# Optimization experiments

Hardware: AMD Instinct MI355X
Metric: run time of the kernel (lower is better)

The kernel has to match this reference:

```python
import jax, jax.numpy as jnp
import numpy as np

NEG_SLOPE = 0.2
CONV3_NUM, CONV1_NUM, POLY_NUM = 3, 5, 4
FEAT_DIM = CONV3_NUM * 84 + CONV1_NUM * 12 + POLY_NUM * 12  # 360
DN = ('NCHW', 'OIHW', 'NCHW')


def leaky_relu(x):
    return jnp.where(x >= 0, x, NEG_SLOPE * x)


def conv3x3(x, feat):
    # per-sample dynamic 3x3 conv: feat[:, :81] -> kernel [3,3,3,3], feat[:, 81:84] -> bias
    B = x.shape[0]
    k = feat[:, :81].reshape(B, 3, 3, 3, 3)
    b = feat[:, 81:84]

    def one(xi, ki, bi):
        y = jax.lax.conv_general_dilated(xi[None], ki, (1, 1), 'SAME', dimension_numbers=DN)[0]
        return y + bi[:, None, None]

    return leaky_relu(jax.vmap(one)(x, k, b))


def conv1x1(x, feat):
    B = x.shape[0]
    k = feat[:, :9].reshape(B, 3, 3, 1, 1)
    b = feat[:, 9:12]

    def one(xi, ki, bi):
        y = jax.lax.conv_general_dilated(xi[None], ki, (1, 1), 'VALID', dimension_numbers=DN)[0]
        return y + bi[:, None, None]

    return leaky_relu(jax.vmap(one)(x, k, b))


def conv_stack(x, feature):
    residual = x
    for i in range(CONV3_NUM):
        x = conv3x3(x, feature[:, i * 84:(i + 1) * 84])
    off = CONV3_NUM * 84
    for i in range(CONV1_NUM):
        x = conv1x1(x, feature[:, off + i * 12:off + (i + 1) * 12])
    return residual + x


def att_map(feat, h_mat, w_mat, xc):
    # product over POLY_NUM of (a*h + b*w + c*x + d)
    att = jnp.ones_like(xc)
    for i in range(POLY_NUM):
        a = feat[:, i * 4 + 0].reshape(-1, 1, 1, 1)
        b = feat[:, i * 4 + 1].reshape(-1, 1, 1, 1)
        c = feat[:, i * 4 + 2].reshape(-1, 1, 1, 1)
        d = feat[:, i * 4 + 3].reshape(-1, 1, 1, 1)
        att = att * (a * h_mat + b * w_mat + c * xc + d)
    return att


def apply_attention(x, feature):
    H, W = x.shape[2], x.shape[3]
    h_mat = (jnp.arange(H, dtype=x.dtype) / H).reshape(1, 1, H, 1)
    w_mat = (jnp.arange(W, dtype=x.dtype) / W).reshape(1, 1, 1, W)
    off = CONV3_NUM * 84 + CONV1_NUM * 12
    atts = [att_map(feature[:, off + c * POLY_NUM * 4: off + (c + 1) * POLY_NUM * 4],
                    h_mat, w_mat, x[:, c:c + 1]) for c in range(3)]  # R, G, B
    att = jnp.concatenate(atts, axis=1)
    return x * (1 + att)


def setup_inputs() -> dict:
    key = jax.random.key(0)
    k1, k2, k3 = jax.random.split(key, 3)
    x = jax.random.uniform(k1, (8, 3, 512, 512), dtype=jnp.float32)
    thumb_x = jax.random.uniform(k2, (8, 3, 64, 64), dtype=jnp.float32)
    Wm = jax.random.normal(k3, (3, FEAT_DIM), dtype=jnp.float32) * 0.05
    bm = jnp.zeros((FEAT_DIM,), dtype=jnp.float32)
    return {"x": x, "thumb_x": thumb_x, "Wm": Wm, "bm": bm}


def reference(x, thumb_x, Wm, bm):
    # meta: GAP over thumbnail -> linear -> per-sample hypernetwork features [B, 360]
    feature = jnp.mean(thumb_x, axis=(2, 3)) @ Wm + bm
    x = conv_stack(x, feature)
    x = apply_attention(x, feature)
    thumb = conv_stack(thumb_x, feature)
    thumb = apply_attention(thumb, feature)
    return (x, thumb)
```

## Files before the change

### kernel.cpp

```cpp
#include <hip/hip_runtime.h>


typedef float v2f __attribute__((ext_vector_type(2)));
#define FMA2(a, b, c) __builtin_elementwise_fma((a), (b), (c))

__device__ __forceinline__ v2f leaky2(v2f v) {
    return __builtin_elementwise_max(v, v * 0.2f);
}

constexpr int STRD = 84;
constexpr int ROWS0 = 22;
constexpr int CHS  = ROWS0 * STRD;
constexpr int BUFSZ = 3 * CHS + 16;

__global__ __launch_bounds__(384) void prep_kernel(
    const float* __restrict__ thumb, const float* __restrict__ Wm,
    const float* __restrict__ bm, float* __restrict__ feat)
{
    const int b = blockIdx.x;
    const int t = threadIdx.x;
    const int ch = t >> 7;
    const int l  = t & 127;
    const float4* p = (const float4*)(thumb + (size_t)b * 3 * 4096);
    float s = 0.f;
#pragma unroll
    for (int k = 0; k < 8; ++k) {
        float4 v = p[ch * 1024 + l + k * 128];
        s += v.x + v.y + v.z + v.w;
    }
    __shared__ float red[384];
    red[t] = s;
    __syncthreads();
    for (int off = 64; off > 0; off >>= 1) {
        if (l < off) red[t] += red[t + off];
        __syncthreads();
    }
    if (t < 360) {
        const float sc = 1.f / 4096.f;
        const float m0 = red[0] * sc, m1 = red[128] * sc, m2 = red[256] * sc;
        feat[b * 360 + t] =
            fmaf(m0, Wm[t], fmaf(m1, Wm[360 + t], fmaf(m2, Wm[720 + t], bm[t])));
    }
}

__device__ __forceinline__ void conv_rows_pk(
    const float* __restrict__ buf, const float* __restrict__ fw,
    int r0, int gx, v2f acc[3][4])
{
    const float b0 = fw[81], b1 = fw[82], b2 = fw[83];
#pragma unroll
    for (int c = 0; c < 4; ++c) {
        v2f i0 = {b0, b0}; v2f i1 = {b1, b1}; v2f i2 = {b2, b2};
        acc[0][c] = i0; acc[1][c] = i1; acc[2][c] = i2;
    }
    const int gA = (gx < 0) ? 0 : gx;
#pragma unroll
    for (int ich = 0; ich < 3; ++ich) {
        float4 QA[4], QB[4], QC[4];
#pragma unroll
        for (int ri = 0; ri < 4; ++ri) {
            const int idx = ich * CHS + (r0 + 2 + ri) * STRD;
            QA[ri] = *(const float4*)&buf[idx + gA];
            QB[ri] = *(const float4*)&buf[idx + gx + 4];
            QC[ri] = *(const float4*)&buf[idx + gx + 8];
        }
#pragma unroll
        for (int dy = 0; dy < 3; ++dy) {
            v2f win[6];
            {
                v2f a = {QA[dy].w, QA[dy + 1].w}; win[0] = a;
                v2f b = {QB[dy].x, QB[dy + 1].x}; win[1] = b;
                v2f c = {QB[dy].y, QB[dy + 1].y}; win[2] = c;
                v2f d = {QB[dy].z, QB[dy + 1].z}; win[3] = d;
                v2f e = {QB[dy].w, QB[dy + 1].w}; win[4] = e;
                v2f f = {QC[dy].x, QC[dy + 1].x}; win[5] = f;
            }
#pragma unroll
            for (int oc = 0; oc < 3; ++oc) {
                const float w0 = fw[oc * 27 + ich * 9 + dy * 3 + 0];
                const float w1 = fw[oc * 27 + ich * 9 + dy * 3 + 1];
                const float w2 = fw[oc * 27 + ich * 9 + dy * 3 + 2];
                v2f W0 = {w0, w0}; v2f W1 = {w1, w1}; v2f W2 = {w2, w2};
#pragma unroll
                for (int c = 0; c < 4; ++c) {
                    acc[oc][c] = FMA2(win[c], W0,
                                 FMA2(win[c + 1], W1,
                                 FMA2(win[c + 2], W2, acc[oc][c])));
                }
            }
        }
    }
}

__device__ __forceinline__ void write_strip_pk(
    float* __restrict__ buf, int r0, int gx, v2f acc[3][4])
{
#pragma unroll
    for (int oc = 0; oc < 3; ++oc) {
        v2f l0 = leaky2(acc[oc][0]);
        v2f l1 = leaky2(acc[oc][1]);
        v2f l2 = leaky2(acc[oc][2]);
        v2f l3 = leaky2(acc[oc][3]);
        float4 ra = make_float4(l0.x, l1.x, l2.x, l3.x);
        float4 rb = make_float4(l0.y, l1.y, l2.y, l3.y);
        *(float4*)&buf[oc * CHS + (r0 + 3) * STRD + gx + 4] = ra;
        *(float4*)&buf[oc * CHS + (r0 + 4) * STRD + gx + 4] = rb;
    }
}

__global__ __launch_bounds__(256, 4) void conv_att_kernel(
    const float* __restrict__ x, const float* __restrict__ thumb,
    const float* __restrict__ feat, float* __restrict__ out)
{
    __shared__ float buf[BUFSZ];

    int id = blockIdx.x;
    const float* src; float* dst; int H, W, b, trow, tcol;
    if (id < 2048) {
        b = id >> 8; const int t = id & 255;
        H = 512; W = 512; trow = (t >> 3) * 16; tcol = (t & 7) * 64;
        src = x; dst = out;
    } else {
        const int i2 = id - 2048;
        b = i2 >> 2; trow = (i2 & 3) * 16; tcol = 0;
        H = 64; W = 64; src = thumb;
        dst = out + (size_t)8 * 3 * 512 * 512;
    }
    const float* fb = feat + b * 360;
    const int tid = threadIdx.x;

    const float* sbg = src + (size_t)b * 3 * H * W;
    for (int q = tid; q < 1056; q += 256) {
        const int c = q / 352;
        const int rem = q - c * 352;
        const int mr = rem >> 4;
        const int k  = rem & 15;
        const int gr = trow + mr - 3;
        const int gc0 = tcol + 4 * k;
        float4 v = make_float4(0.f, 0.f, 0.f, 0.f);
        if ((unsigned)gr < (unsigned)H)
            v = *(const float4*)&sbg[(size_t)c * H * W + (size_t)gr * W + gc0];
        *(float4*)&buf[c * CHS + mr * STRD + 4 * (k + 1)] = v;
    }
    if (tid < 132) {
        const int c = tid / 44;
        const int rem = tid - c * 44;
        const int mr = rem >> 1;
        const int side = rem & 1;
        const int gr = trow + mr - 3;
        const int gc0 = tcol + (side ? 64 : -4);
        const bool rok = (unsigned)gr < (unsigned)H;
        const float* gp = sbg + (size_t)c * H * W + (size_t)(rok ? gr : 0) * W;
        float4 v;
        if (rok && (unsigned)gc0 <= (unsigned)(W - 4)) {
            v = *(const float4*)&gp[gc0];
        } else {
            v.x = (rok && (unsigned)(gc0 + 0) < (unsigned)W) ? gp[gc0 + 0] : 0.f;
            v.y = (rok && (unsigned)(gc0 + 1) < (unsigned)W) ? gp[gc0 + 1] : 0.f;
            v.z = (rok && (unsigned)(gc0 + 2) < (unsigned)W) ? gp[gc0 + 2] : 0.f;
            v.w = (rok && (unsigned)(gc0 + 3) < (unsigned)W) ? gp[gc0 + 3] : 0.f;
        }
        *(float4*)&buf[c * CHS + mr * STRD + (side ? 68 : 0)] = v;
    }
    if (tid < 66) {
        const int c = tid / 22, mr = tid - c * 22;
        *(float4*)&buf[c * CHS + mr * STRD + 72] = make_float4(0.f, 0.f, 0.f, 0.f);
    }
    __syncthreads();

    const bool act1 = tid < 180;
    int s1, gx1;
    if (tid < 160) { s1 = tid >> 4; gx1 = 4 * (tid & 15); }
    else { const int v = tid - 160; s1 = v >> 1; gx1 = (v & 1) ? 64 : -4; }
    v2f acc[3][4];
    if (act1) conv_rows_pk(buf, fb, 2 * s1 - 2, gx1, acc);

    const int s3 = tid >> 4;
    const int gx3 = 4 * (tid & 15);
    v2f res2[3][4];
    if (tid < 128) {
#pragma unroll
        for (int ch = 0; ch < 3; ++ch) {
            float4 ra = *(const float4*)&buf[ch * CHS + (2 * s3 + 3) * STRD + gx3 + 4];
            float4 rb = *(const float4*)&buf[ch * CHS + (2 * s3 + 4) * STRD + gx3 + 4];
            v2f p0 = {ra.x, rb.x}; res2[ch][0] = p0;
            v2f p1 = {ra.y, rb.y}; res2[ch][1] = p1;
            v2f p2 = {ra.z, rb.z}; res2[ch][2] = p2;
            v2f p3 = {ra.w, rb.w}; res2[ch][3] = p3;
        }
    }
    __syncthreads();

    if (act1) write_strip_pk(buf, 2 * s1 - 2, gx1, acc);
    __syncthreads();

    const bool act2 = tid < 162;
    int s2, gx2;
    if (tid < 144) { s2 = tid >> 4; gx2 = 4 * (tid & 15); }
    else { const int v = tid - 144; s2 = v >> 1; gx2 = (v & 1) ? 64 : -4; }
    if (act2) conv_rows_pk(buf, fb + 84, 2 * s2 - 1, gx2, acc);
    __syncthreads();

    if (act2) write_strip_pk(buf, 2 * s2 - 1, gx2, acc);
    __syncthreads();

    if (tid < 128) {
        v2f y[3][4];
        {
            v2f acc3[3][4];
            conv_rows_pk(buf, fb + 168, 2 * s3, gx3, acc3);
#pragma unroll
            for (int oc = 0; oc < 3; ++oc)
#pragma unroll
                for (int c = 0; c < 4; ++c) y[oc][c] = leaky2(acc3[oc][c]);
        }

#pragma unroll
        for (int lay = 0; lay < 5; ++lay) {
            const float* fw = fb + 252 + lay * 12;
            v2f W0 = {fw[0], fw[0]}; v2f W1 = {fw[1], fw[1]}; v2f W2 = {fw[2], fw[2]};
            v2f W3 = {fw[3], fw[3]}; v2f W4 = {fw[4], fw[4]}; v2f W5 = {fw[5], fw[5]};
            v2f W6 = {fw[6], fw[6]}; v2f W7 = {fw[7], fw[7]}; v2f W8 = {fw[8], fw[8]};
            v2f C0 = {fw[9], fw[9]}; v2f C1 = {fw[10], fw[10]}; v2f C2 = {fw[11], fw[11]};
            v2f z0[4], z1[4], z2[4];
#pragma unroll
            for (int c = 0; c < 4; ++c) {
                z0[c] = FMA2(y[0][c], W0, FMA2(y[1][c], W1, FMA2(y[2][c], W2, C0)));
                z1[c] = FMA2(y[0][c], W3, FMA2(y[1][c], W4, FMA2(y[2][c], W5, C1)));
                z2[c] = FMA2(y[0][c], W6, FMA2(y[1][c], W7, FMA2(y[2][c], W8, C2)));
            }
#pragma unroll
            for (int c = 0; c < 4; ++c) {
                y[0][c] = leaky2(z0[c]);
                y[1][c] = leaky2(z1[c]);
                y[2][c] = leaky2(z2[c]);
            }
        }

        const float invH = 1.f / (float)H;
        const float invW = 1.f / (float)W;
        const int gr0 = trow + 2 * s3;
        v2f h2 = {(float)gr0 * invH, (float)(gr0 + 1) * invH};
        const float wb = (float)(tcol + gx3) * invW;
        const v2f one = {1.f, 1.f};
#pragma unroll
        for (int ch = 0; ch < 3; ++ch) {
            const float* fp = fb + 312 + ch * 16;
            v2f PA0 = {fp[0], fp[0]},  PB0 = {fp[1], fp[1]},  PC0 = {fp[2], fp[2]},  PD0 = {fp[3], fp[3]};
            v2f PA1 = {fp[4], fp[4]},  PB1 = {fp[5], fp[5]},  PC1 = {fp[6], fp[6]},  PD1 = {fp[7], fp[7]};
            v2f PA2 = {fp[8], fp[8]},  PB2 = {fp[9], fp[9]},  PC2 = {fp[10], fp[10]}, PD2 = {fp[11], fp[11]};
            v2f PA3 = {fp[12], fp[12]}, PB3 = {fp[13], fp[13]}, PC3 = {fp[14], fp[14]}, PD3 = {fp[15], fp[15]};
            v2f t0 = FMA2(PA0, h2, PD0);
            v2f t1 = FMA2(PA1, h2, PD1);
            v2f t2 = FMA2(PA2, h2, PD2);
            v2f t3 = FMA2(PA3, h2, PD3);
            v2f o[4];
#pragma unroll
            for (int c = 0; c < 4; ++c) {
                const float wcs = wb + (float)c * invW;
                v2f Wc = {wcs, wcs};
                v2f v = y[ch][c] + res2[ch][c];
                v2f a = FMA2(PB0, Wc, FMA2(PC0, v, t0));
                a = a * FMA2(PB1, Wc, FMA2(PC1, v, t1));
                a = a * FMA2(PB2, Wc, FMA2(PC2, v, t2));
                a = a * FMA2(PB3, Wc, FMA2(PC3, v, t3));
                o[c] = v * (one + a);
            }
            float4 ra = make_float4(o[0].x, o[1].x, o[2].x, o[3].x);
            float4 rb = make_float4(o[0].y, o[1].y, o[2].y, o[3].y);
            float* dp = &dst[((size_t)(b * 3 + ch) * H + gr0) * W + tcol + gx3];
            *(float4*)dp = ra;
            *(float4*)(dp + W) = rb;
        }
    }
}

extern "C" void kernel_launch(void* const* d_in, const int* in_sizes, int n_in,
                              void* d_out, int out_size, void* d_ws, size_t ws_size,
                              hipStream_t stream) {
    const float* x = (const float*)d_in[0];
    const float* thumb = (const float*)d_in[1];
    const float* Wm = (const float*)d_in[2];
    const float* bm = (const float*)d_in[3];
    float* out = (float*)d_out;
    float* feat = (float*)d_ws;

    prep_kernel<<<8, 384, 0, stream>>>(thumb, Wm, bm, feat);
    conv_att_kernel<<<2080, 256, 0, stream>>>(x, thumb, feat, out);
}
```

Baseline: 111.8 us.

## Transpose shared-memory tile to column-major with odd stride for paired-row loads

Changes the LDS tile layout from row-major (stride 84) to column-major with an odd column stride of 23. Vertically adjacent pixel pairs become contiguous, so the packed v2f windows load directly with 8-byte accesses instead of being gathered from float4 row loads. The odd stride is meant to spread bank accesses. The cost is that global loads are now scattered into LDS as four scalar stores each, and the number of LDS load instructions per window goes up.

```diff
diff --git a/kernel.cpp b/kernel.cpp
--- a/kernel.cpp
+++ b/kernel.cpp
@@ -8,10 +8,18 @@
     return __builtin_elementwise_max(v, v * 0.2f);
 }
 
-constexpr int STRD = 84;
+__device__ __forceinline__ v2f ldpair(const float* p) {
+    v2f r; __builtin_memcpy(&r, p, 8); return r;
+}
+__device__ __forceinline__ void stpair(float* p, v2f v) {
+    __builtin_memcpy(p, &v, 8);
+}
+
 constexpr int ROWS0 = 22;
-constexpr int CHS  = ROWS0 * STRD;
-constexpr int BUFSZ = 3 * CHS + 16;
+constexpr int NCOLS = 73;
+constexpr int CSTR  = 23;
+constexpr int CHS   = NCOLS * CSTR;
+constexpr int BUFSZ = 3 * CHS + 4;
 
 __global__ __launch_bounds__(384) void prep_kernel(
     const float* __restrict__ thumb, const float* __restrict__ Wm,
@@ -53,28 +61,18 @@
         v2f i0 = {b0, b0}; v2f i1 = {b1, b1}; v2f i2 = {b2, b2};
         acc[0][c] = i0; acc[1][c] = i1; acc[2][c] = i2;
     }
-    const int gA = (gx < 0) ? 0 : gx;
+    const int c0 = (gx < 0) ? 3 : gx + 3;
+    const int rb = r0 + 2;
 #pragma unroll
     for (int ich = 0; ich < 3; ++ich) {
-        float4 QA[4], QB[4], QC[4];
-#pragma unroll
-        for (int ri = 0; ri < 4; ++ri) {
-            const int idx = ich * CHS + (r0 + 2 + ri) * STRD;
-            QA[ri] = *(const float4*)&buf[idx + gA];
-            QB[ri] = *(const float4*)&buf[idx + gx + 4];
-            QC[ri] = *(const float4*)&buf[idx + gx + 8];
-        }
+        const int base = ich * CHS + rb;
 #pragma unroll
         for (int dy = 0; dy < 3; ++dy) {
             v2f win[6];
-            {
-                v2f a = {QA[dy].w, QA[dy + 1].w}; win[0] = a;
-                v2f b = {QB[dy].x, QB[dy + 1].x}; win[1] = b;
-                v2f c = {QB[dy].y, QB[dy + 1].y}; win[2] = c;
-                v2f d = {QB[dy].z, QB[dy + 1].z}; win[3] = d;
-                v2f e = {QB[dy].w, QB[dy + 1].w}; win[4] = e;
-                v2f f = {QC[dy].x, QC[dy + 1].x}; win[5] = f;
-            }
+            win[0] = ldpair(&buf[base + c0 * CSTR + dy]);
+#pragma unroll
+            for (int k = 1; k < 6; ++k)
+                win[k] = ldpair(&buf[base + (gx + 3 + k) * CSTR + dy]);
 #pragma unroll
             for (int oc = 0; oc < 3; ++oc) {
                 const float w0 = fw[oc * 27 + ich * 9 + dy * 3 + 0];
@@ -96,16 +94,11 @@
     float* __restrict__ buf, int r0, int gx, v2f acc[3][4])
 {
 #pragma unroll
-    for (int oc = 0; oc < 3; ++oc) {
-        v2f l0 = leaky2(acc[oc][0]);
-        v2f l1 = leaky2(acc[oc][1]);
-        v2f l2 = leaky2(acc[oc][2]);
-        v2f l3 = leaky2(acc[oc][3]);
-        float4 ra = make_float4(l0.x, l1.x, l2.x, l3.x);
-        float4 rb = make_float4(l0.y, l1.y, l2.y, l3.y);
-        *(float4*)&buf[oc * CHS + (r0 + 3) * STRD + gx + 4] = ra;
-        *(float4*)&buf[oc * CHS + (r0 + 4) * STRD + gx + 4] = rb;
-    }
+    for (int oc = 0; oc < 3; ++oc)
+#pragma unroll
+        for (int c = 0; c < 4; ++c)
+            stpair(&buf[oc * CHS + (gx + 4 + c) * CSTR + (r0 + 3)],
+                   leaky2(acc[oc][c]));
 }
 
 __global__ __launch_bounds__(256, 4) void conv_att_kernel(
@@ -140,7 +133,8 @@
         float4 v = make_float4(0.f, 0.f, 0.f, 0.f);
         if ((unsigned)gr < (unsigned)H)
             v = *(const float4*)&sbg[(size_t)c * H * W + (size_t)gr * W + gc0];
-        *(float4*)&buf[c * CHS + mr * STRD + 4 * (k + 1)] = v;
+        float* bp = &buf[c * CHS + (4 * k + 4) * CSTR + mr];
+        bp[0] = v.x; bp[CSTR] = v.y; bp[2 * CSTR] = v.z; bp[3 * CSTR] = v.w;
     }
     if (tid < 132) {
         const int c = tid / 44;
@@ -160,11 +154,12 @@
             v.z = (rok && (unsigned)(gc0 + 2) < (unsigned)W) ? gp[gc0 + 2] : 0.f;
             v.w = (rok && (unsigned)(gc0 + 3) < (unsigned)W) ? gp[gc0 + 3] : 0.f;
         }
-        *(float4*)&buf[c * CHS + mr * STRD + (side ? 68 : 0)] = v;
+        float* bp = &buf[c * CHS + (side ? 68 : 0) * CSTR + mr];
+        bp[0] = v.x; bp[CSTR] = v.y; bp[2 * CSTR] = v.z; bp[3 * CSTR] = v.w;
     }
     if (tid < 66) {
         const int c = tid / 22, mr = tid - c * 22;
-        *(float4*)&buf[c * CHS + mr * STRD + 72] = make_float4(0.f, 0.f, 0.f, 0.f);
+        buf[c * CHS + 72 * CSTR + mr] = 0.f;
     }
     __syncthreads();
 
@@ -180,14 +175,10 @@
     v2f res2[3][4];
     if (tid < 128) {
 #pragma unroll
-        for (int ch = 0; ch < 3; ++ch) {
-            float4 ra = *(const float4*)&buf[ch * CHS + (2 * s3 + 3) * STRD + gx3 + 4];
-            float4 rb = *(const float4*)&buf[ch * CHS + (2 * s3 + 4) * STRD + gx3 + 4];
-            v2f p0 = {ra.x, rb.x}; res2[ch][0] = p0;
-            v2f p1 = {ra.y, rb.y}; res2[ch][1] = p1;
-            v2f p2 = {ra.z, rb.z}; res2[ch][2] = p2;
-            v2f p3 = {ra.w, rb.w}; res2[ch][3] = p3;
-        }
+        for (int ch = 0; ch < 3; ++ch)
+#pragma unroll
+            for (int c = 0; c < 4; ++c)
+                res2[ch][c] = ldpair(&buf[ch * CHS + (gx3 + 4 + c) * CSTR + (2 * s3 + 3)]);
     }
     __syncthreads();
 
```

After: 111.7 us. About the same (-0.1%).
